# Performance work log

Hardware: AMD Instinct MI355X
Metric: run time of the kernel (lower is better)

Reference implementation:

```python
import jax, jax.numpy as jnp
import numpy as np

MODEL_DIM = 2048
INNER_DIM = 512
NUM_HEADS = 16
FFN_DIM = 8192
MEM_TOKENS = 64
BATCH = 2
SEQ = 2048
EPS = 1e-6


def _rmsnorm(x, w):
    # norm = ||x|| / sqrt(d); out = w * x / (norm + eps)
    norm = jnp.linalg.norm(x, axis=-1, keepdims=True) / np.sqrt(x.shape[-1])
    return w * x / (norm + EPS)


def setup_inputs() -> dict:
    key = jax.random.key(0)
    names_shapes = [
        ("x", (BATCH, SEQ, MODEL_DIM)), ("memory", (BATCH, MEM_TOKENS, MODEL_DIM)),
        ("wq", (MODEL_DIM, MODEL_DIM)), ("wk", (MODEL_DIM, MODEL_DIM)),
        ("wv", (MODEL_DIM, MODEL_DIM)), ("wz", (MODEL_DIM, MODEL_DIM)),
        ("wg", (MODEL_DIM, MODEL_DIM)),
        ("md1", (MODEL_DIM, INNER_DIM)), ("md2", (INNER_DIM, MODEL_DIM)),
        ("mcw", (MODEL_DIM, MODEL_DIM)),
        ("awq", (MODEL_DIM, MODEL_DIM)), ("awk", (MODEL_DIM, MODEL_DIM)),
        ("awv", (MODEL_DIM, MODEL_DIM)), ("awo", (MODEL_DIM, MODEL_DIM)),
        ("f1", (MODEL_DIM, FFN_DIM)), ("f2", (FFN_DIM, MODEL_DIM)),
    ]
    keys = jax.random.split(key, len(names_shapes))
    inp = {}
    for (name, shape), k in zip(names_shapes, keys):
        scale = 1.0 if name in ("x", "memory") else 0.02
        inp[name] = jax.random.normal(k, shape, dtype=jnp.float32) * scale
    for name, dim in [("bq", MODEL_DIM), ("bk", MODEL_DIM), ("bv", MODEL_DIM),
                      ("bz", MODEL_DIM), ("bg", MODEL_DIM), ("mb1", INNER_DIM),
                      ("mb2", MODEL_DIM), ("mcb", MODEL_DIM), ("abq", MODEL_DIM),
                      ("abk", MODEL_DIM), ("abv", MODEL_DIM), ("abo", MODEL_DIM),
                      ("fb1", FFN_DIM), ("fb2", MODEL_DIM)]:
        inp[name] = jnp.zeros((dim,), dtype=jnp.float32)
    inp["n1w"] = jnp.ones((MODEL_DIM,), dtype=jnp.float32)
    inp["n2w"] = jnp.ones((MODEL_DIM,), dtype=jnp.float32)
    return inp


def reference(x, memory, wq, bq, wk, bk, wv, bv, wz, bz, wg, bg, n1w, n2w,
              md1, mb1, md2, mb2, mcw, mcb, awq, abq, awk, abk, awv, abv,
              awo, abo, f1, fb1, f2, fb2):
    B, S, D = x.shape
    H = NUM_HEADS
    dh = D // H

    # 1. projections on RMS-normed input
    xn = _rmsnorm(x, n1w)
    k_ = xn @ wk + bk
    v_ = xn @ wv + bv  # computed as in original (feeds attention path via h_t)
    z = xn @ wz + bz

    # MDI decay gamma: 2-layer decay net + context modulation, sigmoid
    gamma = jax.nn.sigmoid((jax.nn.gelu(z @ md1 + mb1) @ md2 + mb2)
                           + (k_ @ mcw + mcb))

    # 2. associative scan (exponential cumulative product) on contiguous reshape
    g4 = gamma.reshape(B, H, S, dh)  # faithful torch .view semantics
    cumprod = jnp.cumprod(g4, axis=2).reshape(B, S, D)

    # 3-4. core formula: h_t = z_t * sigmoid(W_g h_prev) + gamma * h_prev
    gate = jax.nn.sigmoid(x @ wg + bg)
    h_t = z * gate + gamma * x

    # 5. multi-memory attention: queries from h_t, keys/values from memory bank
    qa = (h_t @ awq + abq).reshape(B, S, H, dh)
    ka = (memory @ awk + abk).reshape(B, -1, H, dh)
    va = (memory @ awv + abv).reshape(B, -1, H, dh)
    scores = jnp.einsum('bshd,bmhd->bhsm', qa, ka) / np.sqrt(dh)
    attn = jax.nn.softmax(scores, axis=-1)
    ctx = jnp.einsum('bhsm,bmhd->bshd', attn, va).reshape(B, S, D)
    mem_context = ctx @ awo + abo

    # 6. residuals (dropout in eval mode = identity)
    x_residual = x + (h_t + mem_context)

    # 7. FFN + residual
    xn2 = _rmsnorm(x_residual, n2w)
    ffn_out = jax.nn.gelu(xn2 @ f1 + fb1) @ f2 + fb2
    output = x_residual + ffn_out
    return output, cumprod
```

## Files before the change

### kernel.cpp

```cpp
#include <hip/hip_runtime.h>
#include <stdint.h>
#include <stddef.h>


#define DEV __device__ __forceinline__

typedef __attribute__((ext_vector_type(8))) short bh8;
typedef __attribute__((ext_vector_type(4))) float f32x4;

typedef __attribute__((address_space(1))) uint32_t gu32;
typedef __attribute__((address_space(3))) uint32_t lu32;

DEV void async16(const void* g, void* l) {
  __builtin_amdgcn_global_load_lds((gu32*)g, (lu32*)l, 16, 0, 0);
}

DEV float b2f(short s) {
  union { float f; uint32_t u; } x;
  x.u = ((uint32_t)(uint16_t)s) << 16;
  return x.f;
}
DEV short f2b(float f) {
  uint32_t u = __float_as_uint(f);
  u += 0x7fffu + ((u >> 16) & 1u);
  return (short)(u >> 16);
}
DEV float sigmoid_f(float x) { return 1.f / (1.f + __expf(-x)); }
DEV float gelu_f(float x) {
  float y = 0.7978845608028654f * (x + 0.044715f * x * x * x);
  float t = 1.f - 2.f / (__expf(2.f * y) + 1.f);
  return 0.5f * x * (1.f + t);
}

template <int EPI>
__global__ __launch_bounds__(256) void gemm_k(
    const short* __restrict__ A, const short* __restrict__ Bt,
    const float* __restrict__ bias, void* Cv,
    const void* aux0, const void* aux1, int M, int N, int K) {
  __shared__ __align__(16) short sA[128 * 32];
  __shared__ __align__(16) short sB[128 * 32];
  const int tid  = threadIdx.x;
  const int lane = tid & 63;
  const int wave = tid >> 6;
  const int q = lane >> 4;
  const int r = lane & 15;
  const int m0 = blockIdx.y * 128;
  const int n0 = blockIdx.x * 128;
  const int wm = (wave >> 1) * 64;
  const int wn = (wave & 1) * 64;

  const int L0 = tid, L1 = 256 + tid;
  const short* gA0 = A + (size_t)(m0 + (L0 >> 2)) * K + (L0 & 3) * 8;
  const short* gA1 = A + (size_t)(m0 + (L1 >> 2)) * K + (L1 & 3) * 8;
  const short* gB0 = Bt + (size_t)(n0 + (L0 >> 2)) * K + (L0 & 3) * 8;
  const short* gB1 = Bt + (size_t)(n0 + (L1 >> 2)) * K + (L1 & 3) * 8;
  short* lA0 = &sA[L0 * 8];
  short* lA1 = &sA[L1 * 8];
  short* lB0 = &sB[L0 * 8];
  short* lB1 = &sB[L1 * 8];

  f32x4 acc[4][4] = {};
  const int nk = K >> 5;
  for (int kt = 0; kt < nk; ++kt) {
    __syncthreads();
    const int kb = kt << 5;
    async16(gA0 + kb, lA0);
    async16(gA1 + kb, lA1);
    async16(gB0 + kb, lB0);
    async16(gB1 + kb, lB1);
    asm volatile("s_waitcnt vmcnt(0)" ::: "memory");
    __syncthreads();
    bh8 af[4], bf[4];
#pragma unroll
    for (int i = 0; i < 4; ++i)
      af[i] = *(const bh8*)&sA[(wm + i * 16 + r) * 32 + q * 8];
#pragma unroll
    for (int j = 0; j < 4; ++j)
      bf[j] = *(const bh8*)&sB[(wn + j * 16 + r) * 32 + q * 8];
#pragma unroll
    for (int i = 0; i < 4; ++i)
#pragma unroll
      for (int j = 0; j < 4; ++j)
        acc[i][j] = __builtin_amdgcn_mfma_f32_16x16x32_bf16(af[i], bf[j], acc[i][j], 0, 0, 0);
  }

#pragma unroll
  for (int j = 0; j < 4; ++j) {
    const int col = n0 + wn + j * 16 + r;
    const float bv = bias[col];
#pragma unroll
    for (int i = 0; i < 4; ++i) {
#pragma unroll
      for (int rr = 0; rr < 4; ++rr) {
        const int row = m0 + wm + i * 16 + q * 4 + rr;
        const size_t idx = (size_t)row * N + col;
        float v = acc[i][j][rr] + bv;
        if constexpr (EPI == 0) {
          ((short*)Cv)[idx] = f2b(v);
        } else if constexpr (EPI == 1) {
          ((short*)Cv)[idx] = f2b(gelu_f(v));
        } else if constexpr (EPI == 2) {
          ((float*)Cv)[idx] = v;
        } else if constexpr (EPI == 3) {
          ((float*)Cv)[idx] = sigmoid_f(v + ((const float*)aux0)[idx]);
        } else if constexpr (EPI == 4) {
          ((float*)Cv)[idx] = v + ((const float*)aux0)[idx] + b2f(((const short*)aux1)[idx]);
        } else {
          ((float*)Cv)[idx] = v + ((const float*)aux0)[idx];
        }
      }
    }
  }
}

__global__ __launch_bounds__(256) void transpose_k(const float* __restrict__ in,
                                                   short* __restrict__ out,
                                                   int R, int C) {
  __shared__ float t[64][68];
  const int tx = threadIdx.x, ty = threadIdx.y;
  const int c0 = blockIdx.x * 64, r0 = blockIdx.y * 64;
#pragma unroll
  for (int yy = 0; yy < 64; yy += 16) {
    const float4 v = *(const float4*)&in[(size_t)(r0 + ty + yy) * C + c0 + tx * 4];
    t[ty + yy][tx * 4 + 0] = v.x;
    t[ty + yy][tx * 4 + 1] = v.y;
    t[ty + yy][tx * 4 + 2] = v.z;
    t[ty + yy][tx * 4 + 3] = v.w;
  }
  __syncthreads();
#pragma unroll
  for (int yy = 0; yy < 64; yy += 16) {
    short4 v;
    v.x = f2b(t[tx * 4 + 0][ty + yy]);
    v.y = f2b(t[tx * 4 + 1][ty + yy]);
    v.z = f2b(t[tx * 4 + 2][ty + yy]);
    v.w = f2b(t[tx * 4 + 3][ty + yy]);
    *(short4*)&out[(size_t)(c0 + ty + yy) * R + r0 + tx * 4] = v;
  }
}

__global__ __launch_bounds__(256) void cvt_k(const float* __restrict__ in,
                                             short* __restrict__ out) {
  const size_t i = ((size_t)blockIdx.x * 256 + threadIdx.x) * 4;
  const float4 v = *(const float4*)(in + i);
  short4 o;
  o.x = f2b(v.x); o.y = f2b(v.y); o.z = f2b(v.z); o.w = f2b(v.w);
  *(short4*)(out + i) = o;
}

__global__ __launch_bounds__(256) void rmsnorm_k(const float* __restrict__ in,
                                                 const float* __restrict__ w,
                                                 short* __restrict__ out) {
  const int row = blockIdx.x;
  const int tid = threadIdx.x;
  const size_t base = (size_t)row * 2048;
  float v[8];
  const float* p = in + base + tid * 8;
#pragma unroll
  for (int i = 0; i < 8; ++i) v[i] = p[i];
  float ss = 0.f;
#pragma unroll
  for (int i = 0; i < 8; ++i) ss += v[i] * v[i];
  for (int off = 32; off; off >>= 1) ss += __shfl_down(ss, off);
  __shared__ float red[4];
  __shared__ float sscale;
  if ((tid & 63) == 0) red[tid >> 6] = ss;
  __syncthreads();
  if (tid == 0) {
    float tot = red[0] + red[1] + red[2] + red[3];
    sscale = 1.f / (sqrtf(tot * (1.f / 2048.f)) + 1e-6f);
  }
  __syncthreads();
  const float scale = sscale;
  short* o = out + base + tid * 8;
#pragma unroll
  for (int i = 0; i < 8; ++i) o[i] = f2b(w[tid * 8 + i] * v[i] * scale);
}

__global__ __launch_bounds__(256) void ht_k(const short* __restrict__ z,
                                            const short* __restrict__ gp,
                                            const float* __restrict__ gamma,
                                            const float* __restrict__ x,
                                            short* __restrict__ ht) {
  const size_t i = ((size_t)blockIdx.x * 256 + threadIdx.x) * 4;
  const short4 z4 = *(const short4*)(z + i);
  const short4 g4 = *(const short4*)(gp + i);
  const float4 x4 = *(const float4*)(x + i);
  const float4 gm = *(const float4*)(gamma + i);
  short4 o;
  o.x = f2b(b2f(z4.x) * sigmoid_f(b2f(g4.x)) + gm.x * x4.x);
  o.y = f2b(b2f(z4.y) * sigmoid_f(b2f(g4.y)) + gm.y * x4.y);
  o.z = f2b(b2f(z4.z) * sigmoid_f(b2f(g4.z)) + gm.z * x4.z);
  o.w = f2b(b2f(z4.w) * sigmoid_f(b2f(g4.w)) + gm.w * x4.w);
  *(short4*)(ht + i) = o;
}

__global__ __launch_bounds__(128) void cumprod1_k(float* __restrict__ gamma,
                                                  float* __restrict__ segprod) {
  const int bx = blockIdx.x;
  const int b = bx >> 7, h = (bx >> 3) & 15, seg = bx & 7;
  size_t base = (size_t)b * 4194304 + (size_t)h * 262144 + (size_t)seg * 256 * 128 + threadIdx.x;
  float acc = 1.f;
  for (int s = 0; s < 256; ++s) {
    acc *= gamma[base + (size_t)s * 128];
    gamma[base + (size_t)s * 128] = acc;
  }
  segprod[(size_t)bx * 128 + threadIdx.x] = acc;
}

__global__ __launch_bounds__(128) void cumprod2_k(const float* __restrict__ gamma,
                                                  const float* __restrict__ segprod,
                                                  float* __restrict__ out) {
  const int bx = blockIdx.x;
  const int b = bx >> 7, h = (bx >> 3) & 15, seg = bx & 7;
  size_t base = (size_t)b * 4194304 + (size_t)h * 262144 + (size_t)seg * 256 * 128 + threadIdx.x;
  float pre = 1.f;
  const size_t sp0 = (size_t)(bx & ~7) * 128 + threadIdx.x;
  for (int t = 0; t < seg; ++t) pre *= segprod[sp0 + (size_t)t * 128];
  for (int s = 0; s < 256; ++s)
    out[base + (size_t)s * 128] = gamma[base + (size_t)s * 128] * pre;
}

__global__ __launch_bounds__(512) void attn_k(const short* __restrict__ qa,
                                              const short* __restrict__ ka,
                                              const short* __restrict__ va,
                                              short* __restrict__ ctx) {
  __shared__ short sk[64][136];
  __shared__ short sv[64][136];
  __shared__ float sq[32][128];
  __shared__ float ss[32][64];
  const int tid = threadIdx.x;
  const int b = blockIdx.z, h = blockIdx.y;
  const int s0 = blockIdx.x * 32;
  const size_t hoff = (size_t)h * 128;
  for (int i = tid; i < 64 * 128; i += 512) {
    int m = i >> 7, d = i & 127;
    sk[m][d] = ka[((size_t)b * 64 + m) * 2048 + hoff + d];
    sv[m][d] = va[((size_t)b * 64 + m) * 2048 + hoff + d];
  }
  for (int i = tid; i < 32 * 128; i += 512) {
    int s = i >> 7, d = i & 127;
    sq[s][d] = b2f(qa[((size_t)b * 2048 + s0 + s) * 2048 + hoff + d]);
  }
  __syncthreads();
  const int g = tid >> 4;
  const int t = tid & 15;
  float sc[4];
#pragma unroll
  for (int mi = 0; mi < 4; ++mi) {
    const int m = mi * 16 + t;
    float a = 0.f;
    for (int d = 0; d < 128; ++d) a += sq[g][d] * b2f(sk[m][d]);
    sc[mi] = a * 0.08838834764831843f;
  }
  float mx = fmaxf(fmaxf(sc[0], sc[1]), fmaxf(sc[2], sc[3]));
#pragma unroll
  for (int off = 8; off; off >>= 1) mx = fmaxf(mx, __shfl_xor(mx, off, 16));
  float sum = 0.f;
#pragma unroll
  for (int mi = 0; mi < 4; ++mi) { sc[mi] = __expf(sc[mi] - mx); sum += sc[mi]; }
#pragma unroll
  for (int off = 8; off; off >>= 1) sum += __shfl_xor(sum, off, 16);
  const float inv = 1.f / sum;
#pragma unroll
  for (int mi = 0; mi < 4; ++mi) ss[g][mi * 16 + t] = sc[mi] * inv;
  __syncthreads();
  const int d0 = t * 8;
  float o[8] = {};
  for (int m = 0; m < 64; ++m) {
    const float wgt = ss[g][m];
#pragma unroll
    for (int i = 0; i < 8; ++i) o[i] += wgt * b2f(sv[m][d0 + i]);
  }
  short* op = ctx + ((size_t)b * 2048 + s0 + g) * 2048 + hoff + d0;
#pragma unroll
  for (int i = 0; i < 8; ++i) op[i] = f2b(o[i]);
}

extern "C" void kernel_launch(void* const* d_in, const int* in_sizes, int n_in,
                              void* d_out, int out_size, void* d_ws, size_t ws_size,
                              hipStream_t stream) {
  (void)in_sizes; (void)n_in; (void)out_size; (void)ws_size;
  const float* x   = (const float*)d_in[0];
  const float* mem = (const float*)d_in[1];
  const float* wk  = (const float*)d_in[3];
  const float* wz  = (const float*)d_in[5];
  const float* wg  = (const float*)d_in[6];
  const float* md1 = (const float*)d_in[7];
  const float* md2 = (const float*)d_in[8];
  const float* mcw = (const float*)d_in[9];
  const float* awq = (const float*)d_in[10];
  const float* awk = (const float*)d_in[11];
  const float* awv = (const float*)d_in[12];
  const float* awo = (const float*)d_in[13];
  const float* f1  = (const float*)d_in[14];
  const float* f2  = (const float*)d_in[15];
  const float* bk  = (const float*)d_in[17];
  const float* bz  = (const float*)d_in[19];
  const float* bg  = (const float*)d_in[20];
  const float* mb1 = (const float*)d_in[21];
  const float* mb2 = (const float*)d_in[22];
  const float* mcb = (const float*)d_in[23];
  const float* abq = (const float*)d_in[24];
  const float* abk = (const float*)d_in[25];
  const float* abv = (const float*)d_in[26];
  const float* abo = (const float*)d_in[27];
  const float* fb1 = (const float*)d_in[28];
  const float* fb2 = (const float*)d_in[29];
  const float* n1w = (const float*)d_in[30];
  const float* n2w = (const float*)d_in[31];

  char* W = (char*)d_ws;
  short* wkT  = (short*)(W + 0);
  short* wzT  = (short*)(W + 8388608);
  short* wgT  = (short*)(W + 16777216);
  short* mcwT = (short*)(W + 25165824);
  short* md1T = (short*)(W + 33554432);
  short* md2T = (short*)(W + 35651584);
  short* awqT = (short*)(W + 37748736);
  short* awkT = (short*)(W + 46137344);
  short* awvT = (short*)(W + 54525952);
  short* awoT = (short*)(W + 62914560);
  short* f1T  = (short*)(W + 71303168);
  short* f2T  = (short*)(W + 104857600);
  char*  big  = W + 138412032;
  short* xn   = (short*)(big + 0);
  short* kk   = (short*)(big + 16777216);
  short* z    = (short*)(big + 33554432);
  short* gpre = (short*)(big + 50331648);
  short* ctx  = kk;
  short* t2   = (short*)big;
  short* t1   = (short*)(W + 205520896);
  float* gamma = (float*)(W + 209715200);
  float* xres  = gamma;
  short* ht   = (short*)(W + 243269632);
  short* qa   = (short*)(W + 260046848);
  short* xn2  = qa;
  short* xb   = (short*)(W + 276824064);
  short* memb = (short*)(W + 293601280);
  short* ka   = (short*)(W + 294125568);
  short* va   = (short*)(W + 294649856);
  float* segprod = (float*)(W + 295174144);

  float* out0 = (float*)d_out;
  float* out1 = out0 + 8388608;

  const dim3 tb16(16, 16);
  transpose_k<<<dim3(32, 32), tb16, 0, stream>>>(wk, wkT, 2048, 2048);
  transpose_k<<<dim3(32, 32), tb16, 0, stream>>>(wz, wzT, 2048, 2048);
  transpose_k<<<dim3(32, 32), tb16, 0, stream>>>(wg, wgT, 2048, 2048);
  transpose_k<<<dim3(32, 32), tb16, 0, stream>>>(mcw, mcwT, 2048, 2048);
  transpose_k<<<dim3(8, 32), tb16, 0, stream>>>(md1, md1T, 2048, 512);
  transpose_k<<<dim3(32, 8), tb16, 0, stream>>>(md2, md2T, 512, 2048);
  transpose_k<<<dim3(32, 32), tb16, 0, stream>>>(awq, awqT, 2048, 2048);
  transpose_k<<<dim3(32, 32), tb16, 0, stream>>>(awk, awkT, 2048, 2048);
  transpose_k<<<dim3(32, 32), tb16, 0, stream>>>(awv, awvT, 2048, 2048);
  transpose_k<<<dim3(32, 32), tb16, 0, stream>>>(awo, awoT, 2048, 2048);
  transpose_k<<<dim3(128, 32), tb16, 0, stream>>>(f1, f1T, 2048, 8192);
  transpose_k<<<dim3(32, 128), tb16, 0, stream>>>(f2, f2T, 8192, 2048);

  cvt_k<<<8192, 256, 0, stream>>>(x, xb);
  cvt_k<<<256, 256, 0, stream>>>(mem, memb);
  rmsnorm_k<<<4096, 256, 0, stream>>>(x, n1w, xn);

  gemm_k<0><<<dim3(16, 32), 256, 0, stream>>>(xn, wkT, bk, kk, nullptr, nullptr, 4096, 2048, 2048);
  gemm_k<0><<<dim3(16, 32), 256, 0, stream>>>(xn, wzT, bz, z, nullptr, nullptr, 4096, 2048, 2048);
  gemm_k<0><<<dim3(16, 32), 256, 0, stream>>>(xb, wgT, bg, gpre, nullptr, nullptr, 4096, 2048, 2048);

  gemm_k<1><<<dim3(4, 32), 256, 0, stream>>>(z, md1T, mb1, t1, nullptr, nullptr, 4096, 512, 2048);
  gemm_k<2><<<dim3(16, 32), 256, 0, stream>>>(t1, md2T, mb2, gamma, nullptr, nullptr, 4096, 2048, 512);
  gemm_k<3><<<dim3(16, 32), 256, 0, stream>>>(kk, mcwT, mcb, gamma, gamma, nullptr, 4096, 2048, 2048);

  ht_k<<<8192, 256, 0, stream>>>(z, gpre, gamma, x, ht);

  cumprod1_k<<<256, 128, 0, stream>>>(gamma, segprod);
  cumprod2_k<<<256, 128, 0, stream>>>(gamma, segprod, out1);

  gemm_k<0><<<dim3(16, 32), 256, 0, stream>>>(ht, awqT, abq, qa, nullptr, nullptr, 4096, 2048, 2048);
  gemm_k<0><<<dim3(16, 1), 256, 0, stream>>>(memb, awkT, abk, ka, nullptr, nullptr, 128, 2048, 2048);
  gemm_k<0><<<dim3(16, 1), 256, 0, stream>>>(memb, awvT, abv, va, nullptr, nullptr, 128, 2048, 2048);

  attn_k<<<dim3(64, 16, 2), 512, 0, stream>>>(qa, ka, va, ctx);

  gemm_k<4><<<dim3(16, 32), 256, 0, stream>>>(ctx, awoT, abo, xres, x, ht, 4096, 2048, 2048);

  rmsnorm_k<<<4096, 256, 0, stream>>>(xres, n2w, xn2);

  gemm_k<1><<<dim3(64, 32), 256, 0, stream>>>(xn2, f1T, fb1, t2, nullptr, nullptr, 4096, 8192, 2048);
  gemm_k<5><<<dim3(16, 32), 256, 0, stream>>>(t2, f2T, fb2, out0, xres, nullptr, 4096, 2048, 8192);
}
```

Measured before the change: 1.504 ms.

## Fuse h_t into gamma GEMM epilogue, batch transposes, group-swizzle GEMM tiles

Adds grouped (swizzled) 1D tile ordering to the GEMM so neighbouring blocks share A/B tiles in L2. Computes h_t inside the sigmoid-gamma GEMM epilogue, which removes the separate ht kernel. Folds the bf16 conversion of x into the first rmsnorm pass, which removes a cvt launch. Merges eight 2048x2048 weight transposes into one launch. The GEMM epilogue now does extra loads, and the index arithmetic adds per-block div/mod work.

```diff
diff --git a/kernel.cpp b/kernel.cpp
--- a/kernel.cpp
+++ b/kernel.cpp
@@ -32,11 +32,12 @@
   return 0.5f * x * (1.f + t);
 }
 
-template <int EPI>
+template <int EPI, int GROUP>
 __global__ __launch_bounds__(256) void gemm_k(
     const short* __restrict__ A, const short* __restrict__ Bt,
     const float* __restrict__ bias, void* Cv,
-    const void* aux0, const void* aux1, int M, int N, int K) {
+    const void* aux0, const void* aux1, const void* aux2, const void* aux3,
+    void* out2, int M, int N, int K) {
   __shared__ __align__(16) short sA[128 * 32];
   __shared__ __align__(16) short sB[128 * 32];
   const int tid  = threadIdx.x;
@@ -44,8 +45,17 @@
   const int wave = tid >> 6;
   const int q = lane >> 4;
   const int r = lane & 15;
-  const int m0 = blockIdx.y * 128;
-  const int n0 = blockIdx.x * 128;
+
+  const int grid_m = M >> 7, grid_n = N >> 7;
+  const int pid = blockIdx.x;
+  const int width = GROUP * grid_n;
+  const int gid = pid / width;
+  const int fm = gid * GROUP;
+  const int gsz = min(grid_m - fm, GROUP);
+  const int rem = pid - gid * width;
+  const int m0 = (fm + rem % gsz) * 128;
+  const int n0 = (rem / gsz) * 128;
+
   const int wm = (wave >> 1) * 64;
   const int wn = (wave & 1) * 64;
 
@@ -102,7 +112,12 @@
         } else if constexpr (EPI == 2) {
           ((float*)Cv)[idx] = v;
         } else if constexpr (EPI == 3) {
-          ((float*)Cv)[idx] = sigmoid_f(v + ((const float*)aux0)[idx]);
+          const float g = sigmoid_f(v + ((const float*)aux0)[idx]);
+          ((float*)Cv)[idx] = g;
+          const float zz = b2f(((const short*)aux1)[idx]);
+          const float gp = b2f(((const short*)aux2)[idx]);
+          const float xx = ((const float*)aux3)[idx];
+          ((short*)out2)[idx] = f2b(zz * sigmoid_f(gp) + g * xx);
         } else if constexpr (EPI == 4) {
           ((float*)Cv)[idx] = v + ((const float*)aux0)[idx] + b2f(((const short*)aux1)[idx]);
         } else {
@@ -139,6 +154,33 @@
   }
 }
 
+struct TP8 { const float* s[8]; short* d[8]; };
+__global__ __launch_bounds__(256) void transpose8_k(TP8 p) {
+  __shared__ float t[64][68];
+  const float* __restrict__ in = p.s[blockIdx.z];
+  short* __restrict__ out = p.d[blockIdx.z];
+  const int tx = threadIdx.x, ty = threadIdx.y;
+  const int c0 = blockIdx.x * 64, r0 = blockIdx.y * 64;
+#pragma unroll
+  for (int yy = 0; yy < 64; yy += 16) {
+    const float4 v = *(const float4*)&in[(size_t)(r0 + ty + yy) * 2048 + c0 + tx * 4];
+    t[ty + yy][tx * 4 + 0] = v.x;
+    t[ty + yy][tx * 4 + 1] = v.y;
+    t[ty + yy][tx * 4 + 2] = v.z;
+    t[ty + yy][tx * 4 + 3] = v.w;
+  }
+  __syncthreads();
+#pragma unroll
+  for (int yy = 0; yy < 64; yy += 16) {
+    short4 v;
+    v.x = f2b(t[tx * 4 + 0][ty + yy]);
+    v.y = f2b(t[tx * 4 + 1][ty + yy]);
+    v.z = f2b(t[tx * 4 + 2][ty + yy]);
+    v.w = f2b(t[tx * 4 + 3][ty + yy]);
+    *(short4*)&out[(size_t)(c0 + ty + yy) * 2048 + r0 + tx * 4] = v;
+  }
+}
+
 __global__ __launch_bounds__(256) void cvt_k(const float* __restrict__ in,
                                              short* __restrict__ out) {
   const size_t i = ((size_t)blockIdx.x * 256 + threadIdx.x) * 4;
@@ -148,9 +190,11 @@
   *(short4*)(out + i) = o;
 }
 
+template <bool RAW>
 __global__ __launch_bounds__(256) void rmsnorm_k(const float* __restrict__ in,
                                                  const float* __restrict__ w,
-                                                 short* __restrict__ out) {
+                                                 short* __restrict__ out,
+                                                 short* __restrict__ raw) {
   const int row = blockIdx.x;
   const int tid = threadIdx.x;
   const size_t base = (size_t)row * 2048;
@@ -158,6 +202,12 @@
   const float* p = in + base + tid * 8;
 #pragma unroll
   for (int i = 0; i < 8; ++i) v[i] = p[i];
+  if constexpr (RAW) {
+    short rw[8];
+#pragma unroll
+    for (int i = 0; i < 8; ++i) rw[i] = f2b(v[i]);
+    *(bh8*)(raw + base + tid * 8) = *(bh8*)rw;
+  }
   float ss = 0.f;
 #pragma unroll
   for (int i = 0; i < 8; ++i) ss += v[i] * v[i];
@@ -175,24 +225,6 @@
   short* o = out + base + tid * 8;
 #pragma unroll
   for (int i = 0; i < 8; ++i) o[i] = f2b(w[tid * 8 + i] * v[i] * scale);
-}
-
-__global__ __launch_bounds__(256) void ht_k(const short* __restrict__ z,
-                                            const short* __restrict__ gp,
-                                            const float* __restrict__ gamma,
-                                            const float* __restrict__ x,
-                                            short* __restrict__ ht) {
-  const size_t i = ((size_t)blockIdx.x * 256 + threadIdx.x) * 4;
-  const short4 z4 = *(const short4*)(z + i);
-  const short4 g4 = *(const short4*)(gp + i);
-  const float4 x4 = *(const float4*)(x + i);
-  const float4 gm = *(const float4*)(gamma + i);
-  short4 o;
-  o.x = f2b(b2f(z4.x) * sigmoid_f(b2f(g4.x)) + gm.x * x4.x);
-  o.y = f2b(b2f(z4.y) * sigmoid_f(b2f(g4.y)) + gm.y * x4.y);
-  o.z = f2b(b2f(z4.z) * sigmoid_f(b2f(g4.z)) + gm.z * x4.z);
-  o.w = f2b(b2f(z4.w) * sigmoid_f(b2f(g4.w)) + gm.w * x4.w);
-  *(short4*)(ht + i) = o;
 }
 
 __global__ __launch_bounds__(128) void cumprod1_k(float* __restrict__ gamma,
@@ -346,46 +378,45 @@
   float* out1 = out0 + 8388608;
 
   const dim3 tb16(16, 16);
-  transpose_k<<<dim3(32, 32), tb16, 0, stream>>>(wk, wkT, 2048, 2048);
-  transpose_k<<<dim3(32, 32), tb16, 0, stream>>>(wz, wzT, 2048, 2048);
-  transpose_k<<<dim3(32, 32), tb16, 0, stream>>>(wg, wgT, 2048, 2048);
-  transpose_k<<<dim3(32, 32), tb16, 0, stream>>>(mcw, mcwT, 2048, 2048);
+  TP8 tp;
+  tp.s[0] = wk;  tp.d[0] = wkT;
+  tp.s[1] = wz;  tp.d[1] = wzT;
+  tp.s[2] = wg;  tp.d[2] = wgT;
+  tp.s[3] = mcw; tp.d[3] = mcwT;
+  tp.s[4] = awq; tp.d[4] = awqT;
+  tp.s[5] = awk; tp.d[5] = awkT;
+  tp.s[6] = awv; tp.d[6] = awvT;
+  tp.s[7] = awo; tp.d[7] = awoT;
+  transpose8_k<<<dim3(32, 32, 8), tb16, 0, stream>>>(tp);
   transpose_k<<<dim3(8, 32), tb16, 0, stream>>>(md1, md1T, 2048, 512);
   transpose_k<<<dim3(32, 8), tb16, 0, stream>>>(md2, md2T, 512, 2048);
-  transpose_k<<<dim3(32, 32), tb16, 0, stream>>>(awq, awqT, 2048, 2048);
-  transpose_k<<<dim3(32, 32), tb16, 0, stream>>>(awk, awkT, 2048, 2048);
-  transpose_k<<<dim3(32, 32), tb16, 0, stream>>>(awv, awvT, 2048, 2048);
-  transpose_k<<<dim3(32, 32), tb16, 0, stream>>>(awo, awoT, 2048, 2048);
   transpose_k<<<dim3(128, 32), tb16, 0, stream>>>(f1, f1T, 2048, 8192);
   transpose_k<<<dim3(32, 128), tb16, 0, stream>>>(f2, f2T, 8192, 2048);
 
-  cvt_k<<<8192, 256, 0, stream>>>(x, xb);
   cvt_k<<<256, 256, 0, stream>>>(mem, memb);
-  rmsnorm_k<<<4096, 256, 0, stream>>>(x, n1w, xn);
-
-  gemm_k<0><<<dim3(16, 32), 256, 0, stream>>>(xn, wkT, bk, kk, nullptr, nullptr, 4096, 2048, 2048);
-  gemm_k<0><<<dim3(16, 32), 256, 0, stream>>>(xn, wzT, bz, z, nullptr, nullptr, 4096, 2048, 2048);
-  gemm_k<0><<<dim3(16, 32), 256, 0, stream>>>(xb, wgT, bg, gpre, nullptr, nullptr, 4096, 2048, 2048);
-
-  gemm_k<1><<<dim3(4, 32), 256, 0, stream>>>(z, md1T, mb1, t1, nullptr, nullptr, 4096, 512, 2048);
-  gemm_k<2><<<dim3(16, 32), 256, 0, stream>>>(t1, md2T, mb2, gamma, nullptr, nullptr, 4096, 2048, 512);
-  gemm_k<3><<<dim3(16, 32), 256, 0, stream>>>(kk, mcwT, mcb, gamma, gamma, nullptr, 4096, 2048, 2048);
-
-  ht_k<<<8192, 256, 0, stream>>>(z, gpre, gamma, x, ht);
+  rmsnorm_k<true><<<4096, 256, 0, stream>>>(x, n1w, xn, xb);
+
+  gemm_k<0, 16><<<512, 256, 0, stream>>>(xn, wkT, bk, kk, nullptr, nullptr, nullptr, nullptr, nullptr, 4096, 2048, 2048);
+  gemm_k<0, 16><<<512, 256, 0, stream>>>(xn, wzT, bz, z, nullptr, nullptr, nullptr, nullptr, nullptr, 4096, 2048, 2048);
+  gemm_k<0, 16><<<512, 256, 0, stream>>>(xb, wgT, bg, gpre, nullptr, nullptr, nullptr, nullptr, nullptr, 4096, 2048, 2048);
+
+  gemm_k<1, 16><<<128, 256, 0, stream>>>(z, md1T, mb1, t1, nullptr, nullptr, nullptr, nullptr, nullptr, 4096, 512, 2048);
+  gemm_k<2, 16><<<512, 256, 0, stream>>>(t1, md2T, mb2, gamma, nullptr, nullptr, nullptr, nullptr, nullptr, 4096, 2048, 512);
+  gemm_k<3, 16><<<512, 256, 0, stream>>>(kk, mcwT, mcb, gamma, gamma, z, gpre, x, ht, 4096, 2048, 2048);
 
   cumprod1_k<<<256, 128, 0, stream>>>(gamma, segprod);
   cumprod2_k<<<256, 128, 0, stream>>>(gamma, segprod, out1);
 
-  gemm_k<0><<<dim3(16, 32), 256, 0, stream>>>(ht, awqT, abq, qa, nullptr, nullptr, 4096, 2048, 2048);
-  gemm_k<0><<<dim3(16, 1), 256, 0, stream>>>(memb, awkT, abk, ka, nullptr, nullptr, 128, 2048, 2048);
-  gemm_k<0><<<dim3(16, 1), 256, 0, stream>>>(memb, awvT, abv, va, nullptr, nullptr, 128, 2048, 2048);
+  gemm_k<0, 16><<<512, 256, 0, stream>>>(ht, awqT, abq, qa, nullptr, nullptr, nullptr, nullptr, nullptr, 4096, 2048, 2048);
+  gemm_k<0, 16><<<16, 256, 0, stream>>>(memb, awkT, abk, ka, nullptr, nullptr, nullptr, nullptr, nullptr, 128, 2048, 2048);
+  gemm_k<0, 16><<<16, 256, 0, stream>>>(memb, awvT, abv, va, nullptr, nullptr, nullptr, nullptr, nullptr, 128, 2048, 2048);
 
   attn_k<<<dim3(64, 16, 2), 512, 0, stream>>>(qa, ka, va, ctx);
 
-  gemm_k<4><<<dim3(16, 32), 256, 0, stream>>>(ctx, awoT, abo, xres, x, ht, 4096, 2048, 2048);
-
-  rmsnorm_k<<<4096, 256, 0, stream>>>(xres, n2w, xn2);
-
-  gemm_k<1><<<dim3(64, 32), 256, 0, stream>>>(xn2, f1T, fb1, t2, nullptr, nullptr, 4096, 8192, 2048);
-  gemm_k<5><<<dim3(16, 32), 256, 0, stream>>>(t2, f2T, fb2, out0, xres, nullptr, 4096, 2048, 8192);
-}
+  gemm_k<4, 16><<<512, 256, 0, stream>>>(ctx, awoT, abo, xres, x, ht, nullptr, nullptr, nullptr, 4096, 2048, 2048);
+
+  rmsnorm_k<false><<<4096, 256, 0, stream>>>(xres, n2w, xn2, nullptr);
+
+  gemm_k<1, 16><<<2048, 256, 0, stream>>>(xn2, f1T, fb1, t2, nullptr, nullptr, nullptr, nullptr, nullptr, 4096, 8192, 2048);
+  gemm_k<5, 8><<<512, 256, 0, stream>>>(t2, f2T, fb2, out0, xres, nullptr, nullptr, nullptr, nullptr, 4096, 2048, 8192);
+}
```

Result: slower. 1.560 ms (+3.7%).
